# Kernel tuning notes

Measured on AMD Instinct MI355X. Metric: run time of the kernel, lower is better.

## Reference

```python
import jax, jax.numpy as jnp
import numpy as np

RES = 320
B = 32

def make_trajectory():
    # Faithful to get_init_trajectory_full: grid points (i,j), zeroed inside the
    # skip bands (i in [140,170] OR j in [120,160]), then shifted by -res/2.
    I, J = np.meshgrid(np.arange(RES), np.arange(RES), indexing='ij')
    pts = np.stack([I, J], axis=-1).astype(np.float32)
    skip = ((I >= 140) & (I <= 170)) | ((J >= 120) & (J <= 160))
    pts[skip] = 0.0
    pts = pts.reshape(-1, 2) - 0.5 * RES
    return jnp.asarray(pts)

def setup_inputs():
    key = jax.random.key(0)
    k_space_input = jax.random.normal(key, (B, 1, RES, RES, 2), dtype=jnp.float32)
    trajectory = make_trajectory()
    return {"k_space_input": k_space_input, "trajectory": trajectory}

def _forward(k_space_input, trajectory):
    H = W = RES
    b = k_space_input.shape[0]
    # [B,1,H,W,2] -> permute(0,1,4,2,3).squeeze(1) -> [B,2,H,W]
    ksp = jnp.transpose(k_space_input[:, 0], (0, 3, 1, 2))
    c = ksp[:, 0] + 1j * ksp[:, 1]                       # [B,H,W] complex k-space

    # --- bilinear grid-sample at trajectory points (zero padding, align_corners=False) ---
    g = trajectory * (2.0 / W)                           # normalize [-res/2,res/2] -> [-1,1]
    x = ((g[:, 0] + 1.0) * W - 1.0) * 0.5                # pixel x (width)
    y = ((g[:, 1] + 1.0) * H - 1.0) * 0.5                # pixel y (height)
    x0f = jnp.floor(x); y0f = jnp.floor(y)
    fx = x - x0f; fy = y - y0f
    x0 = x0f.astype(jnp.int32); y0 = y0f.astype(jnp.int32)
    corners = ((x0,     y0,     (1 - fx) * (1 - fy)),
               (x0 + 1, y0,     fx       * (1 - fy)),
               (x0,     y0 + 1, (1 - fx) * fy),
               (x0 + 1, y0 + 1, fx       * fy))

    def gather(ix, iy):
        valid = (ix >= 0) & (ix < W) & (iy >= 0) & (iy < H)
        v = c[:, jnp.clip(iy, 0, H - 1), jnp.clip(ix, 0, W - 1)]   # [B,N]
        return jnp.where(valid[None, :], v, 0.0)

    sub = sum(gather(ix, iy) * w[None, :] for ix, iy, w in corners)  # [B,N] sampled k-space

    # --- NUFFT adjoint: bilinear gridding (adjoint scatter-add) + centered inverse FFT ---
    grid = jnp.zeros((b, H * W), dtype=sub.dtype)
    for ix, iy, w in corners:
        valid = (ix >= 0) & (ix < W) & (iy >= 0) & (iy < H)
        idx = jnp.clip(iy, 0, H - 1) * W + jnp.clip(ix, 0, W - 1)
        grid = grid.at[:, idx].add(sub * jnp.where(valid, w, 0.0)[None, :])
    kgrid = grid.reshape(b, H, W)
    img = jnp.fft.fftshift(
        jnp.fft.ifft2(jnp.fft.ifftshift(kgrid, axes=(-2, -1)), axes=(-2, -1)),
        axes=(-2, -1)) * (H * W)                          # adjoint DFT = N * centered ifft
    out = jnp.stack([img.real, img.imag], axis=1)         # [B,2,H,W]
    return out[:, None]                                   # unsqueeze(1) -> [B,1,2,H,W]

def reference(k_space_input, trajectory):
    return _forward(k_space_input, trajectory)
```

## Files before the change

### kernel.cpp

```cpp
#include <hip/hip_runtime.h>

#define RES 320
#define CELLS (RES * RES)
#define MDIM 640
#define NCOLS 10240
#define UF 192

#define DEGC 1360.625f

typedef __attribute__((ext_vector_type(8))) short short8;
typedef __attribute__((ext_vector_type(4))) float f32x4;

static __device__ __forceinline__ short f2bf(float f) {
    unsigned u = __builtin_bit_cast(unsigned, f);
    unsigned r = (u + 0x7fffu + ((u >> 16) & 1u)) >> 16;
    return (short)r;
}

#define GLD16(g, l) __builtin_amdgcn_global_load_lds(                        \
    (const __attribute__((address_space(1))) void*)(g),                      \
    (__attribute__((address_space(3))) void*)(l), 16, 0, 0)

__global__ __launch_bounds__(256) void gen_fafb(short* __restrict__ FBf,
                                                short* __restrict__ FAf) {
    int idx = blockIdx.x * 256 + threadIdx.x;
    int mat = idx / (2 * UF * RES);
    int r = idx - mat * (2 * UF * RES);
    int row = r / RES, c = r % RES;
    int plane = row >= UF;
    int n = row - UF * plane;
    float vr = 0.f;
    if (n <= 160) {
        int lo = mat ? 120 : 140, hi = mat ? 160 : 170;
#pragma unroll
        for (int dx = -1; dx <= 1; dx++) {
            int xx = c - dx;
            if (xx < 0 || xx > RES - 1) continue;
            int a0 = (xx < lo || xx > hi) ? 1 : 0;
            int a1 = (xx + 1 <= RES - 1 && (xx + 1 < lo || xx + 1 > hi)) ? 1 : 0;
            float w;
            if (dx == -1) w = (xx >= 1) ? (float)a0 : 0.f;
            else if (dx == 0) w = (float)(a0 + ((xx <= RES - 2) ? a1 : 0));
            else w = (xx <= RES - 2) ? (float)a1 : 0.f;
            if (w != 0.f) {
                int rr = (n * xx) % RES;
                float s, cc;
                sincospif((float)rr * (2.0f / RES), &s, &cc);
                float sign = ((n + xx) & 1) ? -1.0f : 1.0f;
                vr += w * sign * (plane ? s : cc);
            }
        }
        if (mat == 0) vr *= 0.0625f;
    }
    (mat ? FAf : FBf)[r] = f2bf(vr);
}

__global__ __launch_bounds__(256) void gemm1(const short* __restrict__ FBf,
                                             const float2* __restrict__ ksp,
                                             short* __restrict__ T) {
    __shared__ __align__(16) union {
        struct { short At[2][128 * 32]; short Bt[2][128 * 40]; } s;
        float Q[2][64 * 64];
    } sm;
    int tid = threadIdx.x;
    int lane = tid & 63, wave = tid >> 6;
    int wr = wave >> 1, wc = wave & 1;
    int c0 = blockIdx.x * 64;
    int v0 = blockIdx.y * 64;
    int b = c0 / RES, y0b = c0 % RES;
    const float2* kb = ksp + (size_t)b * CELLS;
    int q = lane >> 4, tl = lane & 15;
    int row4 = tid >> 2, ko = (tid & 3) * 8;
    int brow = tid >> 2, bxq = (tid & 3) * 8;
    f32x4 acc[4][4];
#pragma unroll
    for (int i = 0; i < 4; i++)
#pragma unroll
        for (int j = 0; j < 4; j++) acc[i][j] = {0.f, 0.f, 0.f, 0.f};

#define S1A(buf, k0)                                                         \
    {                                                                        \
        GLD16(FBf + (size_t)(v0 + row4) * RES + (k0) + ko,                   \
              sm.s.At[buf] + (size_t)(wave * 64) * 8);                       \
        GLD16(FBf + (size_t)(UF + v0 + row4) * RES + (k0) + ko,              \
              sm.s.At[buf] + (size_t)(256 + wave * 64) * 8);                 \
    }

    float2 bv[8];
#define S1BLOAD(k0)                                                          \
    {                                                                        \
        const float2* src = kb + (size_t)(y0b + brow) * RES + (k0) + bxq;    \
        _Pragma("unroll") for (int e = 0; e < 8; e++) bv[e] = src[e];        \
    }
#define S1BWRITE(buf)                                                        \
    {                                                                        \
        short8 r8, i8;                                                       \
        _Pragma("unroll") for (int e = 0; e < 8; e++) {                      \
            r8[e] = f2bf(bv[e].x);                                           \
            i8[e] = f2bf(bv[e].y);                                           \
        }                                                                    \
        *(short8*)&sm.s.Bt[buf][brow * 40 + bxq] = r8;                       \
        *(short8*)&sm.s.Bt[buf][(64 + brow) * 40 + bxq] = i8;                \
    }

    S1A(0, 0);
    S1BLOAD(0);
    S1BWRITE(0);
    __syncthreads();
    int cur = 0;
    for (int kt = 0; kt < 10; kt++) {
        if (kt < 9) {
            S1A(cur ^ 1, (kt + 1) * 32);
            S1BLOAD((kt + 1) * 32);
        }
        short8 a[4], bf[4];
#pragma unroll
        for (int i = 0; i < 4; i++)
            a[i] = *(const short8*)&sm.s.At[cur][(wr * 64 + i * 16 + tl) * 32 + q * 8];
#pragma unroll
        for (int j = 0; j < 4; j++)
            bf[j] = *(const short8*)&sm.s.Bt[cur][(wc * 64 + j * 16 + tl) * 40 + q * 8];
#pragma unroll
        for (int i = 0; i < 4; i++)
#pragma unroll
            for (int j = 0; j < 4; j++)
                acc[i][j] = __builtin_amdgcn_mfma_f32_16x16x32_bf16(a[i], bf[j], acc[i][j], 0, 0, 0);
        if (kt < 9) S1BWRITE(cur ^ 1);
        __syncthreads();
        cur ^= 1;
    }
    if (wave == 1 || wave == 3) {
        float* dst = sm.Q[wave >> 1];
#pragma unroll
        for (int i = 0; i < 4; i++)
#pragma unroll
            for (int j = 0; j < 4; j++)
#pragma unroll
                for (int t = 0; t < 4; t++)
                    dst[(i * 16 + q * 4 + t) * 64 + j * 16 + tl] = acc[i][j][t];
    }
    __syncthreads();
    if (wave == 0) {
#pragma unroll
        for (int i = 0; i < 4; i++)
#pragma unroll
            for (int j = 0; j < 4; j++)
#pragma unroll
                for (int t = 0; t < 4; t++) {
                    int r = i * 16 + q * 4 + t, cl = j * 16 + tl;
                    int n = v0 + r, y = y0b + cl;
                    float q11 = sm.Q[1][r * 64 + cl];
                    if (n <= 160)
                        T[(size_t)(b * RES + n) * MDIM + y] = f2bf(acc[i][j][t] - q11);
                    if (n >= 1 && n <= 159)
                        T[(size_t)(b * RES + RES - n) * MDIM + y] = f2bf(acc[i][j][t] + q11);
                }
    } else if (wave == 2) {
#pragma unroll
        for (int i = 0; i < 4; i++)
#pragma unroll
            for (int j = 0; j < 4; j++)
#pragma unroll
                for (int t = 0; t < 4; t++) {
                    int r = i * 16 + q * 4 + t, cl = j * 16 + tl;
                    int n = v0 + r, y = y0b + cl;
                    float q01 = sm.Q[0][r * 64 + cl];
                    if (n <= 160)
                        T[(size_t)(b * RES + n) * MDIM + RES + y] = f2bf(q01 + acc[i][j][t]);
                    if (n >= 1 && n <= 159)
                        T[(size_t)(b * RES + RES - n) * MDIM + RES + y] = f2bf(q01 - acc[i][j][t]);
                }
    }
}

__global__ __launch_bounds__(256) void gemm2(const short* __restrict__ T,
                                             const short* __restrict__ FAf,
                                             const float2* __restrict__ ksp,
                                             float* __restrict__ out) {
    __shared__ __align__(16) union {
        struct { short At[2][128 * 32]; short Bt[2][128 * 32]; } s;
        float Q[2][64 * 64];
    } sm;
    int tid = threadIdx.x;
    int lane = tid & 63, wave = tid >> 6;
    int wr = wave >> 1, wc = wave & 1;
    int c0 = blockIdx.x * 64;
    int v0 = blockIdx.y * 64;
    int b = c0 / RES, n0b = c0 % RES;
    int q = lane >> 4, tl = lane & 15;
    int row4 = tid >> 2, ko = (tid & 3) * 8;
    f32x4 acc[4][4];
#pragma unroll
    for (int i = 0; i < 4; i++)
#pragma unroll
        for (int j = 0; j < 4; j++) acc[i][j] = {0.f, 0.f, 0.f, 0.f};

#define S2(buf, k0)                                                          \
    {                                                                        \
        GLD16(FAf + (size_t)(v0 + row4) * RES + (k0) + ko,                   \
              sm.s.At[buf] + (size_t)(wave * 64) * 8);                       \
        GLD16(FAf + (size_t)(UF + v0 + row4) * RES + (k0) + ko,              \
              sm.s.At[buf] + (size_t)(256 + wave * 64) * 8);                 \
        GLD16(T + (size_t)(c0 + row4) * MDIM + (k0) + ko,                    \
              sm.s.Bt[buf] + (size_t)(wave * 64) * 8);                       \
        GLD16(T + (size_t)(c0 + row4) * MDIM + RES + (k0) + ko,              \
              sm.s.Bt[buf] + (size_t)(256 + wave * 64) * 8);                 \
    }

    S2(0, 0);
    __syncthreads();
    int cur = 0;
    for (int kt = 0; kt < 10; kt++) {
        if (kt < 9) S2(cur ^ 1, (kt + 1) * 32);
        short8 a[4], bf[4];
#pragma unroll
        for (int i = 0; i < 4; i++)
            a[i] = *(const short8*)&sm.s.At[cur][(wr * 64 + i * 16 + tl) * 32 + q * 8];
#pragma unroll
        for (int j = 0; j < 4; j++)
            bf[j] = *(const short8*)&sm.s.Bt[cur][(wc * 64 + j * 16 + tl) * 32 + q * 8];
#pragma unroll
        for (int i = 0; i < 4; i++)
#pragma unroll
            for (int j = 0; j < 4; j++)
                acc[i][j] = __builtin_amdgcn_mfma_f32_16x16x32_bf16(a[i], bf[j], acc[i][j], 0, 0, 0);
        __syncthreads();
        cur ^= 1;
    }
    if (wave == 1 || wave == 3) {
        float* dst = sm.Q[wave >> 1];
#pragma unroll
        for (int i = 0; i < 4; i++)
#pragma unroll
            for (int j = 0; j < 4; j++)
#pragma unroll
                for (int t = 0; t < 4; t++)
                    dst[(i * 16 + q * 4 + t) * 64 + j * 16 + tl] = acc[i][j][t];
    }
    __syncthreads();
    float2 g0 = ksp[(size_t)b * CELLS];
    if (wave == 0) {
        float g = DEGC * g0.x;
#pragma unroll
        for (int i = 0; i < 4; i++)
#pragma unroll
            for (int j = 0; j < 4; j++)
#pragma unroll
                for (int t = 0; t < 4; t++) {
                    int r = i * 16 + q * 4 + t, cl = j * 16 + tl;
                    int m = v0 + r, n = n0b + cl;
                    float q11 = sm.Q[1][r * 64 + cl];
                    float sgn = ((m + n) & 1) ? -1.0f : 1.0f;
                    size_t pb = (size_t)(b * 2) * RES;
                    if (m <= 160)
                        out[(pb + m) * RES + n] = (acc[i][j][t] - q11) + sgn * g;
                    if (m >= 1 && m <= 159)
                        out[(pb + RES - m) * RES + n] = (acc[i][j][t] + q11) + sgn * g;
                }
    } else if (wave == 2) {
        float g = DEGC * g0.y;
#pragma unroll
        for (int i = 0; i < 4; i++)
#pragma unroll
            for (int j = 0; j < 4; j++)
#pragma unroll
                for (int t = 0; t < 4; t++) {
                    int r = i * 16 + q * 4 + t, cl = j * 16 + tl;
                    int m = v0 + r, n = n0b + cl;
                    float q01 = sm.Q[0][r * 64 + cl];
                    float sgn = ((m + n) & 1) ? -1.0f : 1.0f;
                    size_t pb = (size_t)(b * 2 + 1) * RES;
                    if (m <= 160)
                        out[(pb + m) * RES + n] = (q01 + acc[i][j][t]) + sgn * g;
                    if (m >= 1 && m <= 159)
                        out[(pb + RES - m) * RES + n] = (q01 - acc[i][j][t]) + sgn * g;
                }
    }
}

extern "C" void kernel_launch(void* const* d_in, const int* in_sizes, int n_in,
                              void* d_out, int out_size, void* d_ws, size_t ws_size,
                              hipStream_t stream) {
    const float2* ksp = (const float2*)d_in[0];

    short* FBf = (short*)d_ws;
    short* FAf = FBf + (size_t)2 * UF * RES;
    short* T = FAf + (size_t)2 * UF * RES;

    gen_fafb<<<960, 256, 0, stream>>>(FBf, FAf);
    gemm1<<<dim3(160, 3), 256, 0, stream>>>(FBf, ksp, T);
    gemm2<<<dim3(160, 3), 256, 0, stream>>>(T, FAf, ksp, (float*)d_out);
}
```

Baseline: 109.4 us.

## Double K-tile depth in both GEMMs with XOR-swizzled LDS and fold FA generation into gemm1

Both GEMM kernels now stage 64-wide K tiles instead of 32, which halves the number of main-loop iterations and barriers. The A and B LDS tiles use an XOR swizzle on the 16-byte chunk index to reduce bank conflicts. Generation of the FA twiddle matrix moves from the separate setup kernel into gemm1, one entry per thread, so the setup kernel only builds FB. The larger tiles double LDS use per block, which may lower occupancy, and gemm1 spends extra sincos work before its main loop.

```diff
diff --git a/kernel.cpp b/kernel.cpp
--- a/kernel.cpp
+++ b/kernel.cpp
@@ -21,12 +21,7 @@
     (const __attribute__((address_space(1))) void*)(g),                      \
     (__attribute__((address_space(3))) void*)(l), 16, 0, 0)
 
-__global__ __launch_bounds__(256) void gen_fafb(short* __restrict__ FBf,
-                                                short* __restrict__ FAf) {
-    int idx = blockIdx.x * 256 + threadIdx.x;
-    int mat = idx / (2 * UF * RES);
-    int r = idx - mat * (2 * UF * RES);
-    int row = r / RES, c = r % RES;
+static __device__ __forceinline__ float fold_entry(int mat, int row, int c) {
     int plane = row >= UF;
     int n = row - UF * plane;
     float vr = 0.f;
@@ -52,14 +47,20 @@
         }
         if (mat == 0) vr *= 0.0625f;
     }
-    (mat ? FAf : FBf)[r] = f2bf(vr);
+    return vr;
+}
+
+__global__ __launch_bounds__(256) void gen_fbf(short* __restrict__ FBf) {
+    int idx = blockIdx.x * 256 + threadIdx.x;
+    FBf[idx] = f2bf(fold_entry(0, idx / RES, idx % RES));
 }
 
 __global__ __launch_bounds__(256) void gemm1(const short* __restrict__ FBf,
                                              const float2* __restrict__ ksp,
-                                             short* __restrict__ T) {
+                                             short* __restrict__ T,
+                                             short* __restrict__ FAf) {
     __shared__ __align__(16) union {
-        struct { short At[2][128 * 32]; short Bt[2][128 * 40]; } s;
+        struct { short At[2][128 * 64]; short Bt[2][128 * 72]; } s;
         float Q[2][64 * 64];
     } sm;
     int tid = threadIdx.x;
@@ -70,8 +71,13 @@
     int b = c0 / RES, y0b = c0 % RES;
     const float2* kb = ksp + (size_t)b * CELLS;
     int q = lane >> 4, tl = lane & 15;
-    int row4 = tid >> 2, ko = (tid & 3) * 8;
-    int brow = tid >> 2, bxq = (tid & 3) * 8;
+    int brow = tid >> 2, bcol0 = (tid & 3) * 16;
+
+    {
+        int gidx = (blockIdx.y * 160 + blockIdx.x) * 256 + tid;
+        FAf[gidx] = f2bf(fold_entry(1, gidx / RES, gidx % RES));
+    }
+
     f32x4 acc[4][4];
 #pragma unroll
     for (int i = 0; i < 4; i++)
@@ -80,27 +86,34 @@
 
 #define S1A(buf, k0)                                                         \
     {                                                                        \
-        GLD16(FBf + (size_t)(v0 + row4) * RES + (k0) + ko,                   \
-              sm.s.At[buf] + (size_t)(wave * 64) * 8);                       \
-        GLD16(FBf + (size_t)(UF + v0 + row4) * RES + (k0) + ko,              \
-              sm.s.At[buf] + (size_t)(256 + wave * 64) * 8);                 \
-    }
-
-    float2 bv[8];
+        _Pragma("unroll")                                                    \
+        for (int p_ = 0; p_ < 4; p_++) {                                     \
+            int idx_ = p_ * 256 + tid;                                       \
+            int row_ = idx_ >> 3, pc_ = idx_ & 7;                            \
+            int lc_ = pc_ ^ (row_ & 7);                                      \
+            int gr_ = v0 + (row_ & 63) + ((row_ >> 6) ? UF : 0);             \
+            GLD16(FBf + (size_t)gr_ * RES + (k0) + lc_ * 8,                  \
+                  sm.s.At[buf] + (size_t)(p_ * 256 + wave * 64) * 8);        \
+        }                                                                    \
+    }
+
+    float2 bv[16];
 #define S1BLOAD(k0)                                                          \
     {                                                                        \
-        const float2* src = kb + (size_t)(y0b + brow) * RES + (k0) + bxq;    \
-        _Pragma("unroll") for (int e = 0; e < 8; e++) bv[e] = src[e];        \
+        const float2* src = kb + (size_t)(y0b + brow) * RES + (k0) + bcol0;  \
+        _Pragma("unroll") for (int e = 0; e < 16; e++) bv[e] = src[e];       \
     }
 #define S1BWRITE(buf)                                                        \
     {                                                                        \
-        short8 r8, i8;                                                       \
+        short8 ra, rb, ia, ib;                                               \
         _Pragma("unroll") for (int e = 0; e < 8; e++) {                      \
-            r8[e] = f2bf(bv[e].x);                                           \
-            i8[e] = f2bf(bv[e].y);                                           \
+            ra[e] = f2bf(bv[e].x);      ia[e] = f2bf(bv[e].y);               \
+            rb[e] = f2bf(bv[8 + e].x);  ib[e] = f2bf(bv[8 + e].y);           \
         }                                                                    \
-        *(short8*)&sm.s.Bt[buf][brow * 40 + bxq] = r8;                       \
-        *(short8*)&sm.s.Bt[buf][(64 + brow) * 40 + bxq] = i8;                \
+        *(short8*)&sm.s.Bt[buf][brow * 72 + bcol0] = ra;                     \
+        *(short8*)&sm.s.Bt[buf][brow * 72 + bcol0 + 8] = rb;                 \
+        *(short8*)&sm.s.Bt[buf][(64 + brow) * 72 + bcol0] = ia;              \
+        *(short8*)&sm.s.Bt[buf][(64 + brow) * 72 + bcol0 + 8] = ib;          \
     }
 
     S1A(0, 0);
@@ -108,24 +121,33 @@
     S1BWRITE(0);
     __syncthreads();
     int cur = 0;
-    for (int kt = 0; kt < 10; kt++) {
-        if (kt < 9) {
-            S1A(cur ^ 1, (kt + 1) * 32);
-            S1BLOAD((kt + 1) * 32);
+    for (int kt = 0; kt < 5; kt++) {
+        if (kt < 4) {
+            S1A(cur ^ 1, (kt + 1) * 64);
+            S1BLOAD((kt + 1) * 64);
         }
-        short8 a[4], bf[4];
-#pragma unroll
-        for (int i = 0; i < 4; i++)
-            a[i] = *(const short8*)&sm.s.At[cur][(wr * 64 + i * 16 + tl) * 32 + q * 8];
+        short8 a[4][2], bf[4][2];
+#pragma unroll
+        for (int i = 0; i < 4; i++)
+#pragma unroll
+            for (int ks = 0; ks < 2; ks++)
+                a[i][ks] = *(const short8*)&sm.s.At[cur][
+                    (wr * 64 + i * 16 + tl) * 64 + ((ks * 4 + q) ^ (tl & 7)) * 8];
 #pragma unroll
         for (int j = 0; j < 4; j++)
-            bf[j] = *(const short8*)&sm.s.Bt[cur][(wc * 64 + j * 16 + tl) * 40 + q * 8];
-#pragma unroll
-        for (int i = 0; i < 4; i++)
-#pragma unroll
-            for (int j = 0; j < 4; j++)
-                acc[i][j] = __builtin_amdgcn_mfma_f32_16x16x32_bf16(a[i], bf[j], acc[i][j], 0, 0, 0);
-        if (kt < 9) S1BWRITE(cur ^ 1);
+#pragma unroll
+            for (int ks = 0; ks < 2; ks++)
+                bf[j][ks] = *(const short8*)&sm.s.Bt[cur][
+                    (wc * 64 + j * 16 + tl) * 72 + ks * 32 + q * 8];
+#pragma unroll
+        for (int i = 0; i < 4; i++)
+#pragma unroll
+            for (int j = 0; j < 4; j++)
+#pragma unroll
+                for (int ks = 0; ks < 2; ks++)
+                    acc[i][j] = __builtin_amdgcn_mfma_f32_16x16x32_bf16(
+                        a[i][ks], bf[j][ks], acc[i][j], 0, 0, 0);
+        if (kt < 4) S1BWRITE(cur ^ 1);
         __syncthreads();
         cur ^= 1;
     }
@@ -178,7 +200,7 @@
                                              const float2* __restrict__ ksp,
                                              float* __restrict__ out) {
     __shared__ __align__(16) union {
-        struct { short At[2][128 * 32]; short Bt[2][128 * 32]; } s;
+        struct { short At[2][128 * 64]; short Bt[2][128 * 64]; } s;
         float Q[2][64 * 64];
     } sm;
     int tid = threadIdx.x;
@@ -188,42 +210,54 @@
     int v0 = blockIdx.y * 64;
     int b = c0 / RES, n0b = c0 % RES;
     int q = lane >> 4, tl = lane & 15;
-    int row4 = tid >> 2, ko = (tid & 3) * 8;
     f32x4 acc[4][4];
 #pragma unroll
     for (int i = 0; i < 4; i++)
 #pragma unroll
         for (int j = 0; j < 4; j++) acc[i][j] = {0.f, 0.f, 0.f, 0.f};
 
-#define S2(buf, k0)                                                          \
+#define S2(buf, k0)                                                         \
     {                                                                        \
-        GLD16(FAf + (size_t)(v0 + row4) * RES + (k0) + ko,                   \
-              sm.s.At[buf] + (size_t)(wave * 64) * 8);                       \
-        GLD16(FAf + (size_t)(UF + v0 + row4) * RES + (k0) + ko,              \
-              sm.s.At[buf] + (size_t)(256 + wave * 64) * 8);                 \
-        GLD16(T + (size_t)(c0 + row4) * MDIM + (k0) + ko,                    \
-              sm.s.Bt[buf] + (size_t)(wave * 64) * 8);                       \
-        GLD16(T + (size_t)(c0 + row4) * MDIM + RES + (k0) + ko,              \
-              sm.s.Bt[buf] + (size_t)(256 + wave * 64) * 8);                 \
+        _Pragma("unroll")                                                    \
+        for (int p_ = 0; p_ < 4; p_++) {                                     \
+            int idx_ = p_ * 256 + tid;                                       \
+            int row_ = idx_ >> 3, pc_ = idx_ & 7;                            \
+            int lc_ = pc_ ^ (row_ & 7);                                      \
+            int gra_ = v0 + (row_ & 63) + ((row_ >> 6) ? UF : 0);            \
+            GLD16(FAf + (size_t)gra_ * RES + (k0) + lc_ * 8,                 \
+                  sm.s.At[buf] + (size_t)(p_ * 256 + wave * 64) * 8);        \
+            GLD16(T + (size_t)(c0 + (row_ & 63)) * MDIM +                    \
+                      ((row_ >> 6) ? RES : 0) + (k0) + lc_ * 8,              \
+                  sm.s.Bt[buf] + (size_t)(p_ * 256 + wave * 64) * 8);        \
+        }                                                                    \
     }
 
     S2(0, 0);
     __syncthreads();
     int cur = 0;
-    for (int kt = 0; kt < 10; kt++) {
-        if (kt < 9) S2(cur ^ 1, (kt + 1) * 32);
-        short8 a[4], bf[4];
-#pragma unroll
-        for (int i = 0; i < 4; i++)
-            a[i] = *(const short8*)&sm.s.At[cur][(wr * 64 + i * 16 + tl) * 32 + q * 8];
+    for (int kt = 0; kt < 5; kt++) {
+        if (kt < 4) S2(cur ^ 1, (kt + 1) * 64);
+        short8 a[4][2], bf[4][2];
+#pragma unroll
+        for (int i = 0; i < 4; i++)
+#pragma unroll
+            for (int ks = 0; ks < 2; ks++)
+                a[i][ks] = *(const short8*)&sm.s.At[cur][
+                    (wr * 64 + i * 16 + tl) * 64 + ((ks * 4 + q) ^ (tl & 7)) * 8];
 #pragma unroll
         for (int j = 0; j < 4; j++)
-            bf[j] = *(const short8*)&sm.s.Bt[cur][(wc * 64 + j * 16 + tl) * 32 + q * 8];
-#pragma unroll
-        for (int i = 0; i < 4; i++)
-#pragma unroll
-            for (int j = 0; j < 4; j++)
-                acc[i][j] = __builtin_amdgcn_mfma_f32_16x16x32_bf16(a[i], bf[j], acc[i][j], 0, 0, 0);
+#pragma unroll
+            for (int ks = 0; ks < 2; ks++)
+                bf[j][ks] = *(const short8*)&sm.s.Bt[cur][
+                    (wc * 64 + j * 16 + tl) * 64 + ((ks * 4 + q) ^ (tl & 7)) * 8];
+#pragma unroll
+        for (int i = 0; i < 4; i++)
+#pragma unroll
+            for (int j = 0; j < 4; j++)
+#pragma unroll
+                for (int ks = 0; ks < 2; ks++)
+                    acc[i][j] = __builtin_amdgcn_mfma_f32_16x16x32_bf16(
+                        a[i][ks], bf[j][ks], acc[i][j], 0, 0, 0);
         __syncthreads();
         cur ^= 1;
     }
@@ -287,7 +321,7 @@
     short* FAf = FBf + (size_t)2 * UF * RES;
     short* T = FAf + (size_t)2 * UF * RES;
 
-    gen_fafb<<<960, 256, 0, stream>>>(FBf, FAf);
-    gemm1<<<dim3(160, 3), 256, 0, stream>>>(FBf, ksp, T);
+    gen_fbf<<<480, 256, 0, stream>>>(FBf);
+    gemm1<<<dim3(160, 3), 256, 0, stream>>>(FBf, ksp, T, FAf);
     gemm2<<<dim3(160, 3), 256, 0, stream>>>(T, FAf, ksp, (float*)d_out);
 }
```

After: 110.6 us. Within noise of the previous version (+1.1%).
